# Kernel tuning notes

Hardware: AMD Instinct MI355X
Metric: run time of the kernel (lower is better)

Reference implementation:

```python
import jax, jax.numpy as jnp
import numpy as np

NV, NE, H, P = 50000, 10000, 256, 400000

def setup_inputs() -> dict:
    key = jax.random.key(0)
    ks = jax.random.split(key, 16)
    s = 1.0 / np.sqrt(H)
    return {
        "v": jax.random.normal(ks[0], (NV, H), jnp.float32),
        "e": jax.random.normal(ks[1], (NE, H), jnp.float32),
        "W_v2e_w": jax.random.normal(ks[2], (H, H), jnp.float32) * s,
        "W_v2e_b": jnp.zeros((H,), jnp.float32),
        "W_e2v_w": jax.random.normal(ks[3], (H, H), jnp.float32) * s,
        "W_e2v_b": jnp.zeros((H,), jnp.float32),
        "n_weight": jax.random.uniform(ks[4], (NV, 1), jnp.float32),
        "e_weight": jax.random.uniform(ks[5], (NE, 1), jnp.float32),
        "n_reg_weight": jax.random.uniform(ks[6], (P, 1), jnp.float32),
        "e_reg_weight": jax.random.uniform(ks[7], (P, 1), jnp.float32),
        "e_reg_sum": jax.random.uniform(ks[8], (NE, 1), jnp.float32) + 1.0,  # positive normalizer
        "n_reg_sum": jax.random.uniform(ks[9], (NV, 1), jnp.float32) + 1.0,
        "pairs_v": jax.random.randint(ks[10], (P,), 0, NV, jnp.int32),  # ve_lists[:,0]
        "eidx": jax.random.randint(ks[11], (P,), 0, NE, jnp.int32),
        "pairs_e": jax.random.randint(ks[12], (P,), 0, NE, jnp.int32),  # ve_lists[:,1]
        "vidx": jax.random.randint(ks[13], (P,), 0, NV, jnp.int32),
    }

def reference(v, e, W_v2e_w, W_v2e_b, W_e2v_w, W_e2v_b, n_weight, e_weight,
              n_reg_weight, e_reg_weight, e_reg_sum, n_reg_sum,
              pairs_v, eidx, pairs_e, vidx):
    # v2e: dense transform on vertices, gather per incidence, scatter-add into edges
    ve = jax.nn.relu(v @ W_v2e_w.T + W_v2e_b)            # [NV,H]
    v_acc = v * n_weight                                 # v *= n_weight * v_fac(=1)
    msg_ve = (ve * n_weight)[pairs_v] * n_reg_weight     # [P,H]
    e_out = e.at[eidx].add(msg_ve) / e_reg_sum           # [NE,H]
    # e2v: dense transform on edges, gather per incidence, scatter-add into vertices
    ev = jax.nn.relu(e_out @ W_e2v_w.T + W_e2v_b)        # [NE,H]
    msg_ev = (ev * e_weight)[pairs_e] * e_reg_weight     # [P,H]
    v_out = v_acc.at[vidx].add(msg_ev) / n_reg_sum       # [NV,H]
    return v_out, e_out
```

## Files before the change

kernel.cpp:

```cpp
#include <hip/hip_runtime.h>
#include <stdint.h>

#define NV 50000
#define NE 10000
#define HD 256
#define NP 400000

#define SE 88
#define SV 36

#define NCH 128
#define CHP (NP / NCH)
#define NW  15000
#define NWE 2500
#define NWV 12500

#define PREP_HBLK NCH
#define PREP_WBLK 16

typedef short short8 __attribute__((ext_vector_type(8)));
typedef short short4v __attribute__((ext_vector_type(4)));
typedef float f32x4 __attribute__((ext_vector_type(4)));

__device__ __forceinline__ short f2bf(float f) {
    unsigned int u = __builtin_bit_cast(unsigned int, f);
    u += 0x7FFFu + ((u >> 16) & 1u);
    return (short)(u >> 16);
}
__device__ __forceinline__ float bf2f(short s) {
    unsigned int u = ((unsigned int)(unsigned short)s) << 16;
    return __builtin_bit_cast(float, u);
}

__global__ __launch_bounds__(1024) void prep_kernel(
    const float* __restrict__ W1, const float* __restrict__ W2,
    const int* __restrict__ eidx, const int* __restrict__ vidx,
    short* __restrict__ W_bf,
    int* __restrict__ cnt8)
{
    __shared__ int h[NW];
    int b = blockIdx.x;
    int tid = threadIdx.x;
    if (b < PREP_HBLK) {
        for (int w = tid; w < NW; w += 1024) h[w] = 0;
        __syncthreads();
        int base = b * CHP;
        for (int k = tid; k < CHP; k += 1024) {
            int p = base + k;
            int er = eidx[p];
            atomicAdd((unsigned*)&h[er >> 2], 1u << ((er & 3) * 8));
            int rv = 10000 + vidx[p];
            atomicAdd((unsigned*)&h[rv >> 2], 1u << ((rv & 3) * 8));
        }
        __syncthreads();
        for (int w = tid; w < NW; w += 1024) cnt8[b * NW + w] = h[w];
    } else {
        size_t i = (size_t)(b - PREP_HBLK) * 8192 + (size_t)tid * 8;
        const float* src = (i < 65536) ? (W1 + i) : (W2 + (i - 65536));
        float4 a0 = *(const float4*)src;
        float4 a1 = *(const float4*)(src + 4);
        short8 s;
        s[0] = f2bf(a0.x); s[1] = f2bf(a0.y); s[2] = f2bf(a0.z); s[3] = f2bf(a0.w);
        s[4] = f2bf(a1.x); s[5] = f2bf(a1.y); s[6] = f2bf(a1.z); s[7] = f2bf(a1.w);
        *(short8*)(W_bf + i) = s;
    }
}

__global__ __launch_bounds__(256) void scan_kernel(
    int* __restrict__ cnt8, int* __restrict__ cnt_e, int* __restrict__ cnt_v)
{
    int w = blockIdx.x * 256 + threadIdx.x;
    if (w >= NW) return;
    unsigned acc = 0;
#pragma unroll 8
    for (int c = 0; c < NCH; ++c) {
        unsigned x = (unsigned)cnt8[c * NW + w];
        cnt8[c * NW + w] = (int)acc;
        acc += x;
    }
    int r0 = w * 4;
    int4 t;
    t.x = acc & 0xFF; t.y = (acc >> 8) & 0xFF; t.z = (acc >> 16) & 0xFF; t.w = acc >> 24;
    if (r0 < 10000) *(int4*)&cnt_e[r0] = t;
    else            *(int4*)&cnt_v[r0 - 10000] = t;
}

__global__ __launch_bounds__(1024) void place_kernel(
    const int* __restrict__ eidx, const int* __restrict__ vidx,
    const int* __restrict__ pairs_v, const int* __restrict__ n_reg_w_bits,
    const int* __restrict__ pairs_e, const int* __restrict__ e_reg_w_bits,
    const int* __restrict__ cnt8,
    int2* __restrict__ bkt_e, int2* __restrict__ bkt_v)
{
    __shared__ int h[NWV];
    int b = blockIdx.x;
    int tid = threadIdx.x;
    if (b < NCH) {
        int c = b;
        for (int w = tid; w < NWE; w += 1024) h[w] = cnt8[c * NW + w];
        __syncthreads();
        int base = c * CHP;
        for (int k = tid; k < CHP; k += 1024) {
            int p = base + k;
            int er = eidx[p];
            unsigned old = atomicAdd((unsigned*)&h[er >> 2], 1u << ((er & 3) * 8));
            int s = (old >> ((er & 3) * 8)) & 0xFF;
            if (s < SE) bkt_e[er * SE + s] = make_int2(pairs_v[p], n_reg_w_bits[p]);
        }
    } else {
        int c = b - NCH;
        for (int w = tid; w < NWV; w += 1024) h[w] = cnt8[c * NW + NWE + w];
        __syncthreads();
        int base = c * CHP;
        for (int k = tid; k < CHP; k += 1024) {
            int p = base + k;
            int vr = vidx[p];
            unsigned old = atomicAdd((unsigned*)&h[vr >> 2], 1u << ((vr & 3) * 8));
            int s = (old >> ((vr & 3) * 8)) & 0xFF;
            if (s < SV) bkt_v[vr * SV + s] = make_int2(pairs_e[p], e_reg_w_bits[p]);
        }
    }
}

__global__ __launch_bounds__(256) void gemm_rs(
    const void* __restrict__ Av, int a_bf,
    const short* __restrict__ Wb,
    const float* __restrict__ bias,
    const float* __restrict__ rowscale,
    short* __restrict__ out,
    int M)
{
    __shared__ short Ws[64 * 256];
    const int tid  = threadIdx.x;
    const int lane = tid & 63;
    const int wv   = tid >> 6;
    const int m16  = lane & 15;
    const int quad = lane >> 4;
    const int arow = (wv << 4) + m16;
    const int row0 = blockIdx.x * 64;
    int gr0 = row0 + arow;
    int gr  = gr0 < M ? gr0 : M - 1;

    short8 a_frag[8];
    if (a_bf) {
        const short* asrc = (const short*)Av + (size_t)gr * HD + (quad << 3);
#pragma unroll
        for (int ks = 0; ks < 8; ++ks)
            a_frag[ks] = *(const short8*)(asrc + (ks << 5));
    } else {
        const float* asrc = (const float*)Av + (size_t)gr * HD + (quad << 3);
#pragma unroll
        for (int ks = 0; ks < 8; ++ks) {
            float4 a0 = *(const float4*)(asrc + (ks << 5));
            float4 a1 = *(const float4*)(asrc + (ks << 5) + 4);
            short8 ap;
            ap[0] = f2bf(a0.x); ap[1] = f2bf(a0.y); ap[2] = f2bf(a0.z); ap[3] = f2bf(a0.w);
            ap[4] = f2bf(a1.x); ap[5] = f2bf(a1.y); ap[6] = f2bf(a1.z); ap[7] = f2bf(a1.w);
            a_frag[ks] = ap;
        }
    }

    for (int ct = 0; ct < 4; ++ct) {
        __syncthreads();
#pragma unroll
        for (int it = 0; it < 8; ++it) {
            int cl = it * 256 + tid;
            int r  = cl >> 5;
            int c  = cl & 31;
            short8 wp = *(const short8*)(Wb + (size_t)((ct << 6) + r) * HD + (c << 3));
            *(short8*)&Ws[(r << 8) + ((c ^ (r & 7)) << 3)] = wp;
        }
        __syncthreads();

        f32x4 acc[4];
#pragma unroll
        for (int nt = 0; nt < 4; ++nt) acc[nt] = (f32x4){0.f, 0.f, 0.f, 0.f};

#pragma unroll
        for (int ks = 0; ks < 8; ++ks) {
            int c = (ks << 2) + quad;
#pragma unroll
            for (int nt = 0; nt < 4; ++nt) {
                int brow = (nt << 4) + m16;
                short8 bfr = *(const short8*)&Ws[(brow << 8) + ((c ^ (m16 & 7)) << 3)];
                acc[nt] = __builtin_amdgcn_mfma_f32_16x16x32_bf16(a_frag[ks], bfr, acc[nt], 0, 0, 0);
            }
        }

#pragma unroll
        for (int r = 0; r < 4; ++r) {
            int row = row0 + (wv << 4) + (quad << 2) + r;
            if (row < M) {
                float rs = rowscale[row];
#pragma unroll
                for (int nt = 0; nt < 4; ++nt) {
                    int col = (ct << 6) + (nt << 4) + m16;
                    float val = acc[nt][r] + bias[col];
                    val = fmaxf(val, 0.0f) * rs;
                    out[(size_t)row * HD + col] = f2bf(val);
                }
            }
        }
    }
}

__device__ __forceinline__ void gather_win(
    const short* __restrict__ msg, int src, int wb, int cnt, int lane,
    float4& A, float4& B)
{
    int j = 0;
    for (; j + 8 <= cnt; j += 8) {
        int s0 = __shfl(src, j),     s1 = __shfl(src, j + 1);
        int s2 = __shfl(src, j + 2), s3 = __shfl(src, j + 3);
        int s4 = __shfl(src, j + 4), s5 = __shfl(src, j + 5);
        int s6 = __shfl(src, j + 6), s7 = __shfl(src, j + 7);
        float w0 = __builtin_bit_cast(float, __shfl(wb, j));
        float w1 = __builtin_bit_cast(float, __shfl(wb, j + 1));
        float w2 = __builtin_bit_cast(float, __shfl(wb, j + 2));
        float w3 = __builtin_bit_cast(float, __shfl(wb, j + 3));
        float w4 = __builtin_bit_cast(float, __shfl(wb, j + 4));
        float w5 = __builtin_bit_cast(float, __shfl(wb, j + 5));
        float w6 = __builtin_bit_cast(float, __shfl(wb, j + 6));
        float w7 = __builtin_bit_cast(float, __shfl(wb, j + 7));
        short4v m0 = *(const short4v*)(msg + ((size_t)s0 << 8) + (lane << 2));
        short4v m1 = *(const short4v*)(msg + ((size_t)s1 << 8) + (lane << 2));
        short4v m2 = *(const short4v*)(msg + ((size_t)s2 << 8) + (lane << 2));
        short4v m3 = *(const short4v*)(msg + ((size_t)s3 << 8) + (lane << 2));
        short4v m4 = *(const short4v*)(msg + ((size_t)s4 << 8) + (lane << 2));
        short4v m5 = *(const short4v*)(msg + ((size_t)s5 << 8) + (lane << 2));
        short4v m6 = *(const short4v*)(msg + ((size_t)s6 << 8) + (lane << 2));
        short4v m7 = *(const short4v*)(msg + ((size_t)s7 << 8) + (lane << 2));
        A.x += bf2f(m0[0]) * w0; A.y += bf2f(m0[1]) * w0;
        A.z += bf2f(m0[2]) * w0; A.w += bf2f(m0[3]) * w0;
        B.x += bf2f(m1[0]) * w1; B.y += bf2f(m1[1]) * w1;
        B.z += bf2f(m1[2]) * w1; B.w += bf2f(m1[3]) * w1;
        A.x += bf2f(m2[0]) * w2; A.y += bf2f(m2[1]) * w2;
        A.z += bf2f(m2[2]) * w2; A.w += bf2f(m2[3]) * w2;
        B.x += bf2f(m3[0]) * w3; B.y += bf2f(m3[1]) * w3;
        B.z += bf2f(m3[2]) * w3; B.w += bf2f(m3[3]) * w3;
        A.x += bf2f(m4[0]) * w4; A.y += bf2f(m4[1]) * w4;
        A.z += bf2f(m4[2]) * w4; A.w += bf2f(m4[3]) * w4;
        B.x += bf2f(m5[0]) * w5; B.y += bf2f(m5[1]) * w5;
        B.z += bf2f(m5[2]) * w5; B.w += bf2f(m5[3]) * w5;
        A.x += bf2f(m6[0]) * w6; A.y += bf2f(m6[1]) * w6;
        A.z += bf2f(m6[2]) * w6; A.w += bf2f(m6[3]) * w6;
        B.x += bf2f(m7[0]) * w7; B.y += bf2f(m7[1]) * w7;
        B.z += bf2f(m7[2]) * w7; B.w += bf2f(m7[3]) * w7;
    }
    for (; j + 2 <= cnt; j += 2) {
        int s0 = __shfl(src, j), s1 = __shfl(src, j + 1);
        float w0 = __builtin_bit_cast(float, __shfl(wb, j));
        float w1 = __builtin_bit_cast(float, __shfl(wb, j + 1));
        short4v m0 = *(const short4v*)(msg + ((size_t)s0 << 8) + (lane << 2));
        short4v m1 = *(const short4v*)(msg + ((size_t)s1 << 8) + (lane << 2));
        A.x += bf2f(m0[0]) * w0; A.y += bf2f(m0[1]) * w0;
        A.z += bf2f(m0[2]) * w0; A.w += bf2f(m0[3]) * w0;
        B.x += bf2f(m1[0]) * w1; B.y += bf2f(m1[1]) * w1;
        B.z += bf2f(m1[2]) * w1; B.w += bf2f(m1[3]) * w1;
    }
    if (j < cnt) {
        int s0 = __shfl(src, j);
        float w0 = __builtin_bit_cast(float, __shfl(wb, j));
        short4v m0 = *(const short4v*)(msg + ((size_t)s0 << 8) + (lane << 2));
        A.x += bf2f(m0[0]) * w0; A.y += bf2f(m0[1]) * w0;
        A.z += bf2f(m0[2]) * w0; A.w += bf2f(m0[3]) * w0;
    }
}

__global__ __launch_bounds__(256) void gather_e(
    const short* __restrict__ msg,
    const int2* __restrict__ bkt,
    const int* __restrict__ cnt,
    const float* __restrict__ e_in, const float* __restrict__ reg_sum,
    float* __restrict__ out, short* __restrict__ out_bf)
{
    int r    = (blockIdx.x << 2) + (threadIdx.x >> 6);
    int lane = threadIdx.x & 63;
    int i0 = r * SE;
    int2 q = bkt[i0 + lane];
    int n = cnt[r]; n = n < SE ? n : SE;
    float4 A = ((const float4*)(e_in + (size_t)r * HD))[lane];
    float4 B = {0.f, 0.f, 0.f, 0.f};
    float inv = 1.0f / reg_sum[r];
    int n0 = n < 64 ? n : 64;
    gather_win(msg, q.x, q.y, n0, lane, A, B);
    if (n > 64) {
        int2 q2 = make_int2(0, 0);
        if (lane < SE - 64) q2 = bkt[i0 + 64 + lane];
        gather_win(msg, q2.x, q2.y, n - 64, lane, A, B);
    }
    float4 acc;
    acc.x = (A.x + B.x) * inv; acc.y = (A.y + B.y) * inv;
    acc.z = (A.z + B.z) * inv; acc.w = (A.w + B.w) * inv;
    ((float4*)(out + (size_t)r * HD))[lane] = acc;
    if (out_bf) {
        short4v s;
        s[0] = f2bf(acc.x); s[1] = f2bf(acc.y); s[2] = f2bf(acc.z); s[3] = f2bf(acc.w);
        *(short4v*)(out_bf + (size_t)r * HD + (lane << 2)) = s;
    }
}

__global__ __launch_bounds__(256) void gather_v(
    const short* __restrict__ msg,
    const int2* __restrict__ bkt,
    const int* __restrict__ cnt,
    const float* __restrict__ v_f32,
    const float* __restrict__ n_w,
    const float* __restrict__ reg_sum, float* __restrict__ out)
{
    int r    = (blockIdx.x << 2) + (threadIdx.x >> 6);
    int lane = threadIdx.x & 63;
    int i0 = r * SV;
    int2 q = bkt[i0 + lane];
    int n = cnt[r]; n = n < SV ? n : SV;
    float nw = n_w[r];
    float inv = 1.0f / reg_sum[r];
    float4 a = ((const float4*)(v_f32 + (size_t)r * HD))[lane];
    float4 A; A.x = a.x * nw; A.y = a.y * nw; A.z = a.z * nw; A.w = a.w * nw;
    float4 B = {0.f, 0.f, 0.f, 0.f};
    gather_win(msg, q.x, q.y, n, lane, A, B);
    float4 acc;
    acc.x = (A.x + B.x) * inv; acc.y = (A.y + B.y) * inv;
    acc.z = (A.z + B.z) * inv; acc.w = (A.w + B.w) * inv;
    ((float4*)(out + (size_t)r * HD))[lane] = acc;
}

extern "C" void kernel_launch(void* const* d_in, const int* in_sizes, int n_in,
                              void* d_out, int out_size, void* d_ws, size_t ws_size,
                              hipStream_t stream) {
    const float* v   = (const float*)d_in[0];
    const float* e   = (const float*)d_in[1];
    const float* W1  = (const float*)d_in[2];
    const float* b1  = (const float*)d_in[3];
    const float* W2  = (const float*)d_in[4];
    const float* b2  = (const float*)d_in[5];
    const float* n_weight     = (const float*)d_in[6];
    const float* e_weight     = (const float*)d_in[7];
    const float* n_reg_weight = (const float*)d_in[8];
    const float* e_reg_weight = (const float*)d_in[9];
    const float* e_reg_sum    = (const float*)d_in[10];
    const float* n_reg_sum    = (const float*)d_in[11];
    const int* pairs_v = (const int*)d_in[12];
    const int* eidx    = (const int*)d_in[13];
    const int* pairs_e = (const int*)d_in[14];
    const int* vidx    = (const int*)d_in[15];

    float* out      = (float*)d_out;
    float* v_region = out;
    float* e_region = out + (size_t)NV * HD;

    char* ws = (char*)d_ws;
    size_t o = 0;
    short* msg     = (short*)(ws + o); o += (size_t)NV * HD * 2;
    int2*  bkt_e   = (int2*)(ws + o);  o += ((size_t)NE * SE + 64) * 8;
    int2*  bkt_v   = (int2*)(ws + o);  o += ((size_t)NV * SV + 64) * 8;
    short* W_bf    = (short*)(ws + o); o += (size_t)2 * 65536 * 2;
    int*   cnt8    = (int*)(ws + o);
    short* e_bf    = (short*)(ws + o); o += (size_t)NCH * NW * 4;
    int*   cnt_e   = (int*)(ws + o);   o += (size_t)NE * 4;
    int*   cnt_v   = (int*)(ws + o);   o += (size_t)NV * 4;

    prep_kernel<<<PREP_HBLK + PREP_WBLK, 1024, 0, stream>>>(
        W1, W2, eidx, vidx, W_bf, cnt8);
    scan_kernel<<<(NW + 255) / 256, 256, 0, stream>>>(cnt8, cnt_e, cnt_v);
    place_kernel<<<2 * NCH, 1024, 0, stream>>>(
        eidx, vidx, pairs_v, (const int*)n_reg_weight,
        pairs_e, (const int*)e_reg_weight, cnt8, bkt_e, bkt_v);

    gemm_rs<<<(NV + 63) / 64, 256, 0, stream>>>(
        (const void*)v, 0, W_bf, b1, n_weight, msg, NV);
    gather_e<<<NE / 4, 256, 0, stream>>>(msg, bkt_e, cnt_e,
        e, e_reg_sum, e_region, e_bf);
    gemm_rs<<<(NE + 63) / 64, 256, 0, stream>>>(
        (const void*)e_bf, 1, W_bf + 65536, b2, e_weight, msg, NE);
    gather_v<<<NV / 4, 256, 0, stream>>>(msg, bkt_v, cnt_v,
        v, n_weight, n_reg_sum, v_region);
}
```

Baseline: 264.1 us.

## Fuse vertex GEMM into bucket placement kernel and process two rows per wave in gather_v

The first dense transform (v @ W1) now runs as extra 1024-thread blocks inside the placement kernel, so bucket construction and the vertex GEMM share one launch and can overlap on the device. The GEMM blocks reuse the shared-memory histogram buffer as the weight tile and handle 256 rows each. gather_v now has each wave process two rows, which gives more independent loads in flight per wave. gemm_rs is reduced to a bf16-input-only path. The costs are larger GEMM blocks with 1024 threads, which may lower occupancy, and more register pressure in gather_v.

```diff
diff --git a/kernel.cpp b/kernel.cpp
--- a/kernel.cpp
+++ b/kernel.cpp
@@ -17,6 +17,7 @@
 
 #define PREP_HBLK NCH
 #define PREP_WBLK 16
+#define GB1 ((NV + 255) / 256)
 
 typedef short short8 __attribute__((ext_vector_type(8)));
 typedef short short4v __attribute__((ext_vector_type(4)));
@@ -85,45 +86,113 @@
     else            *(int4*)&cnt_v[r0 - 10000] = t;
 }
 
-__global__ __launch_bounds__(1024) void place_kernel(
+__global__ __launch_bounds__(1024) void mid_kernel(
     const int* __restrict__ eidx, const int* __restrict__ vidx,
     const int* __restrict__ pairs_v, const int* __restrict__ n_reg_w_bits,
     const int* __restrict__ pairs_e, const int* __restrict__ e_reg_w_bits,
     const int* __restrict__ cnt8,
-    int2* __restrict__ bkt_e, int2* __restrict__ bkt_v)
-{
-    __shared__ int h[NWV];
+    int2* __restrict__ bkt_e, int2* __restrict__ bkt_v,
+    const float* __restrict__ v, const short* __restrict__ Wb,
+    const float* __restrict__ bias, const float* __restrict__ rowscale,
+    short* __restrict__ msg)
+{
+    __shared__ int sm[NWV];
     int b = blockIdx.x;
     int tid = threadIdx.x;
     if (b < NCH) {
         int c = b;
-        for (int w = tid; w < NWE; w += 1024) h[w] = cnt8[c * NW + w];
+        for (int w = tid; w < NWE; w += 1024) sm[w] = cnt8[c * NW + w];
         __syncthreads();
         int base = c * CHP;
         for (int k = tid; k < CHP; k += 1024) {
             int p = base + k;
             int er = eidx[p];
-            unsigned old = atomicAdd((unsigned*)&h[er >> 2], 1u << ((er & 3) * 8));
+            unsigned old = atomicAdd((unsigned*)&sm[er >> 2], 1u << ((er & 3) * 8));
             int s = (old >> ((er & 3) * 8)) & 0xFF;
             if (s < SE) bkt_e[er * SE + s] = make_int2(pairs_v[p], n_reg_w_bits[p]);
         }
-    } else {
+    } else if (b < 2 * NCH) {
         int c = b - NCH;
-        for (int w = tid; w < NWV; w += 1024) h[w] = cnt8[c * NW + NWE + w];
+        for (int w = tid; w < NWV; w += 1024) sm[w] = cnt8[c * NW + NWE + w];
         __syncthreads();
         int base = c * CHP;
         for (int k = tid; k < CHP; k += 1024) {
             int p = base + k;
             int vr = vidx[p];
-            unsigned old = atomicAdd((unsigned*)&h[vr >> 2], 1u << ((vr & 3) * 8));
+            unsigned old = atomicAdd((unsigned*)&sm[vr >> 2], 1u << ((vr & 3) * 8));
             int s = (old >> ((vr & 3) * 8)) & 0xFF;
             if (s < SV) bkt_v[vr * SV + s] = make_int2(pairs_e[p], e_reg_w_bits[p]);
         }
+    } else {
+        short* Ws = (short*)sm;
+        const int lane = tid & 63;
+        const int wv   = tid >> 6;
+        const int m16  = lane & 15;
+        const int quad = lane >> 4;
+        const int arow = (wv << 4) + m16;
+        const int row0 = (b - 2 * NCH) * 256;
+        int gr0 = row0 + arow;
+        int gr  = gr0 < NV ? gr0 : NV - 1;
+
+        short8 a_frag[8];
+        const float* asrc = v + (size_t)gr * HD + (quad << 3);
+#pragma unroll
+        for (int ks = 0; ks < 8; ++ks) {
+            float4 a0 = *(const float4*)(asrc + (ks << 5));
+            float4 a1 = *(const float4*)(asrc + (ks << 5) + 4);
+            short8 ap;
+            ap[0] = f2bf(a0.x); ap[1] = f2bf(a0.y); ap[2] = f2bf(a0.z); ap[3] = f2bf(a0.w);
+            ap[4] = f2bf(a1.x); ap[5] = f2bf(a1.y); ap[6] = f2bf(a1.z); ap[7] = f2bf(a1.w);
+            a_frag[ks] = ap;
+        }
+
+        for (int ct = 0; ct < 4; ++ct) {
+            __syncthreads();
+#pragma unroll
+            for (int it = 0; it < 2; ++it) {
+                int cl = it * 1024 + tid;
+                int r  = cl >> 5;
+                int c  = cl & 31;
+                short8 wp = *(const short8*)(Wb + (size_t)((ct << 6) + r) * HD + (c << 3));
+                *(short8*)&Ws[(r << 8) + ((c ^ (r & 7)) << 3)] = wp;
+            }
+            __syncthreads();
+
+            f32x4 acc[4];
+#pragma unroll
+            for (int nt = 0; nt < 4; ++nt) acc[nt] = (f32x4){0.f, 0.f, 0.f, 0.f};
+
+#pragma unroll
+            for (int ks = 0; ks < 8; ++ks) {
+                int c = (ks << 2) + quad;
+#pragma unroll
+                for (int nt = 0; nt < 4; ++nt) {
+                    int brow = (nt << 4) + m16;
+                    short8 bfr = *(const short8*)&Ws[(brow << 8) + ((c ^ (m16 & 7)) << 3)];
+                    acc[nt] = __builtin_amdgcn_mfma_f32_16x16x32_bf16(a_frag[ks], bfr, acc[nt], 0, 0, 0);
+                }
+            }
+
+#pragma unroll
+            for (int r = 0; r < 4; ++r) {
+                int row = row0 + (wv << 4) + (quad << 2) + r;
+                if (row < NV) {
+                    float rs = rowscale[row];
+#pragma unroll
+                    for (int nt = 0; nt < 4; ++nt) {
+                        int col = (ct << 6) + (nt << 4) + m16;
+                        float val = acc[nt][r] + bias[col];
+                        val = fmaxf(val, 0.0f) * rs;
+                        msg[(size_t)row * HD + col] = f2bf(val);
+                    }
+                }
+            }
+        }
     }
 }
 
 __global__ __launch_bounds__(256) void gemm_rs(
-    const void* __restrict__ Av, int a_bf,
+    const short* __restrict__ Ab,
     const short* __restrict__ Wb,
     const float* __restrict__ bias,
     const float* __restrict__ rowscale,
@@ -142,23 +211,10 @@
     int gr  = gr0 < M ? gr0 : M - 1;
 
     short8 a_frag[8];
-    if (a_bf) {
-        const short* asrc = (const short*)Av + (size_t)gr * HD + (quad << 3);
-#pragma unroll
-        for (int ks = 0; ks < 8; ++ks)
-            a_frag[ks] = *(const short8*)(asrc + (ks << 5));
-    } else {
-        const float* asrc = (const float*)Av + (size_t)gr * HD + (quad << 3);
-#pragma unroll
-        for (int ks = 0; ks < 8; ++ks) {
-            float4 a0 = *(const float4*)(asrc + (ks << 5));
-            float4 a1 = *(const float4*)(asrc + (ks << 5) + 4);
-            short8 ap;
-            ap[0] = f2bf(a0.x); ap[1] = f2bf(a0.y); ap[2] = f2bf(a0.z); ap[3] = f2bf(a0.w);
-            ap[4] = f2bf(a1.x); ap[5] = f2bf(a1.y); ap[6] = f2bf(a1.z); ap[7] = f2bf(a1.w);
-            a_frag[ks] = ap;
-        }
-    }
+    const short* asrc = Ab + (size_t)gr * HD + (quad << 3);
+#pragma unroll
+    for (int ks = 0; ks < 8; ++ks)
+        a_frag[ks] = *(const short8*)(asrc + (ks << 5));
 
     for (int ct = 0; ct < 4; ++ct) {
         __syncthreads();
@@ -308,21 +364,32 @@
     const float* __restrict__ n_w,
     const float* __restrict__ reg_sum, float* __restrict__ out)
 {
-    int r    = (blockIdx.x << 2) + (threadIdx.x >> 6);
+    int wid  = threadIdx.x >> 6;
     int lane = threadIdx.x & 63;
-    int i0 = r * SV;
-    int2 q = bkt[i0 + lane];
-    int n = cnt[r]; n = n < SV ? n : SV;
-    float nw = n_w[r];
-    float inv = 1.0f / reg_sum[r];
-    float4 a = ((const float4*)(v_f32 + (size_t)r * HD))[lane];
-    float4 A; A.x = a.x * nw; A.y = a.y * nw; A.z = a.z * nw; A.w = a.w * nw;
-    float4 B = {0.f, 0.f, 0.f, 0.f};
-    gather_win(msg, q.x, q.y, n, lane, A, B);
-    float4 acc;
-    acc.x = (A.x + B.x) * inv; acc.y = (A.y + B.y) * inv;
-    acc.z = (A.z + B.z) * inv; acc.w = (A.w + B.w) * inv;
-    ((float4*)(out + (size_t)r * HD))[lane] = acc;
+    int r0 = (blockIdx.x << 3) + (wid << 1);
+    int r1 = r0 + 1;
+    int i0 = r0 * SV, i1 = r1 * SV;
+    int2 q0 = bkt[i0 + lane];
+    int2 q1 = bkt[i1 + lane];
+    int n0 = cnt[r0]; n0 = n0 < SV ? n0 : SV;
+    int n1 = cnt[r1]; n1 = n1 < SV ? n1 : SV;
+    float nw0 = n_w[r0], nw1 = n_w[r1];
+    float inv0 = 1.0f / reg_sum[r0], inv1 = 1.0f / reg_sum[r1];
+    float4 a0 = ((const float4*)(v_f32 + (size_t)r0 * HD))[lane];
+    float4 a1 = ((const float4*)(v_f32 + (size_t)r1 * HD))[lane];
+    float4 A0, B0 = {0.f, 0.f, 0.f, 0.f};
+    float4 A1, B1 = {0.f, 0.f, 0.f, 0.f};
+    A0.x = a0.x * nw0; A0.y = a0.y * nw0; A0.z = a0.z * nw0; A0.w = a0.w * nw0;
+    A1.x = a1.x * nw1; A1.y = a1.y * nw1; A1.z = a1.z * nw1; A1.w = a1.w * nw1;
+    gather_win(msg, q0.x, q0.y, n0, lane, A0, B0);
+    gather_win(msg, q1.x, q1.y, n1, lane, A1, B1);
+    float4 o0, o1;
+    o0.x = (A0.x + B0.x) * inv0; o0.y = (A0.y + B0.y) * inv0;
+    o0.z = (A0.z + B0.z) * inv0; o0.w = (A0.w + B0.w) * inv0;
+    o1.x = (A1.x + B1.x) * inv1; o1.y = (A1.y + B1.y) * inv1;
+    o1.z = (A1.z + B1.z) * inv1; o1.w = (A1.w + B1.w) * inv1;
+    ((float4*)(out + (size_t)r0 * HD))[lane] = o0;
+    ((float4*)(out + (size_t)r1 * HD))[lane] = o1;
 }
 
 extern "C" void kernel_launch(void* const* d_in, const int* in_sizes, int n_in,
@@ -363,16 +430,15 @@
     prep_kernel<<<PREP_HBLK + PREP_WBLK, 1024, 0, stream>>>(
         W1, W2, eidx, vidx, W_bf, cnt8);
     scan_kernel<<<(NW + 255) / 256, 256, 0, stream>>>(cnt8, cnt_e, cnt_v);
-    place_kernel<<<2 * NCH, 1024, 0, stream>>>(
+    mid_kernel<<<2 * NCH + GB1, 1024, 0, stream>>>(
         eidx, vidx, pairs_v, (const int*)n_reg_weight,
-        pairs_e, (const int*)e_reg_weight, cnt8, bkt_e, bkt_v);
-
-    gemm_rs<<<(NV + 63) / 64, 256, 0, stream>>>(
-        (const void*)v, 0, W_bf, b1, n_weight, msg, NV);
+        pairs_e, (const int*)e_reg_weight, cnt8, bkt_e, bkt_v,
+        v, W_bf, b1, n_weight, msg);
+
     gather_e<<<NE / 4, 256, 0, stream>>>(msg, bkt_e, cnt_e,
         e, e_reg_sum, e_region, e_bf);
     gemm_rs<<<(NE + 63) / 64, 256, 0, stream>>>(
-        (const void*)e_bf, 1, W_bf + 65536, b2, e_weight, msg, NE);
-    gather_v<<<NV / 4, 256, 0, stream>>>(msg, bkt_v, cnt_v,
+        e_bf, W_bf + 65536, b2, e_weight, msg, NE);
+    gather_v<<<NV / 8, 256, 0, stream>>>(msg, bkt_v, cnt_v,
         v, n_weight, n_reg_sum, v_region);
 }
```

After: 254.2 us. 3.7% less time.
